# Performance work log

Measured on AMD Instinct MI355X. Metric: run time of the kernel, lower is better.

Reference implementation:

```python
import jax, jax.numpy as jnp
import numpy as np

B, D = 8192, 128
MARGIN = 0.1
N_CLASSES, N_GROUPS = 64, 8


def setup_inputs() -> dict:
    key = jax.random.key(0)
    k1, k2, k3 = jax.random.split(key, 3)
    embeddings = jax.random.normal(k1, (B, D), dtype=jnp.float32)
    labels = jax.random.randint(k2, (B,), 0, N_CLASSES, dtype=jnp.int64)
    groups = jax.random.randint(k3, (B,), 0, N_GROUPS, dtype=jnp.int64)
    return {"embeddings": embeddings, "labels": labels, "groups": groups}


def reference(embeddings, labels, groups):
    # cosine metric: L2-normalize rows (torch F.normalize eps=1e-12)
    norm = jnp.maximum(jnp.linalg.norm(embeddings, axis=1, keepdims=True), 1e-12)
    x = embeddings / norm
    dist = 1.0 - jnp.matmul(x, x.T)                      # [B, B]

    n = embeddings.shape[0]
    eye = jnp.eye(n, dtype=bool)
    same_label = labels[:, None] == labels[None, :]       # [B, B]
    pos_mask = same_label & ~eye
    neg_mask = ~same_label
    neg_sg_mask = neg_mask & (groups[:, None] == groups[None, :])

    BIG = jnp.float32(1e9)
    # hardest positive per row (masked max), hardest negative per row (masked min)
    dist_ap = jnp.max(jnp.where(pos_mask, dist, -BIG), axis=1)
    dist_an_sg = jnp.min(jnp.where(neg_sg_mask, dist, BIG), axis=1)
    dist_an_all = jnp.min(jnp.where(neg_mask, dist, BIG), axis=1)

    has_pos = jnp.any(pos_mask, axis=1)
    has_neg_sg = jnp.any(neg_sg_mask, axis=1)
    has_neg = jnp.any(neg_mask, axis=1)

    # fallback: same-group negatives preferred, else any negative
    dist_an = jnp.where(has_neg_sg, dist_an_sg, dist_an_all)

    loss = jax.nn.relu(dist_ap - dist_an + MARGIN)        # [B]
    # original only averages strictly-positive losses over valid anchors
    include = has_pos & has_neg & (loss > 0)
    cnt = jnp.sum(include.astype(jnp.float32))
    total = jnp.sum(jnp.where(include, loss, 0.0))
    final = jnp.where(cnt > 0, total / jnp.maximum(cnt, 1.0), 0.0)
    final = jnp.where(jnp.isnan(final), 0.0, final)
    return final
```

## Files before the change

### kernel.cpp

```cpp
#include <hip/hip_runtime.h>
#include <math.h>

#define NB 8192
#define DK 128
#define SPLITJ 16
#define JSPAN (NB / SPLITJ)
#define NJT (JSPAN / 32)
#define GRID_MINE ((NB / 128) * SPLITJ)

typedef __attribute__((ext_vector_type(8))) short short8;
typedef __attribute__((ext_vector_type(16))) float float16;

__device__ inline unsigned short f2bf(float f) {
    unsigned int x = __float_as_uint(f);
    unsigned int r = (x + 0x7fffu + ((x >> 16) & 1u)) >> 16;
    return (unsigned short)r;
}

__device__ inline unsigned enc_f(float f) {
    unsigned u = __float_as_uint(f);
    return ((int)u < 0) ? ~u : (u | 0x80000000u);
}
__device__ inline float dec_f(unsigned u) {
    unsigned b = (u & 0x80000000u) ? (u & 0x7fffffffu) : ~u;
    return __uint_as_float(b);
}

__global__ void prep_kernel(const float* __restrict__ emb, const int* __restrict__ labels,
                            const int* __restrict__ groups, short8* __restrict__ frag,
                            int* __restrict__ meta, unsigned* __restrict__ apu,
                            unsigned* __restrict__ anu, int* __restrict__ ticket) {
    const int t   = blockIdx.x;
    const int tid = threadIdx.x;
    const int r   = tid >> 3;
    const int ks  = tid & 7;
    const int row = t * 32 + r;

    const float4* src = (const float4*)(emb + (size_t)row * DK + ks * 16);
    float4 q[4];
    float ss = 0.0f;
#pragma unroll
    for (int u = 0; u < 4; u++) {
        q[u] = src[u];
        ss += q[u].x * q[u].x + q[u].y * q[u].y + q[u].z * q[u].z + q[u].w * q[u].w;
    }
#pragma unroll
    for (int off = 4; off; off >>= 1) ss += __shfl_xor(ss, off, 64);
    float inv = 1.0f / fmaxf(sqrtf(ss), 1e-12f);

    unsigned short h[16];
#pragma unroll
    for (int u = 0; u < 4; u++) {
        h[u * 4 + 0] = f2bf(q[u].x * inv);
        h[u * 4 + 1] = f2bf(q[u].y * inv);
        h[u * 4 + 2] = f2bf(q[u].z * inv);
        h[u * 4 + 3] = f2bf(q[u].w * inv);
    }
    short8 lo, hi;
#pragma unroll
    for (int u = 0; u < 8; u++) { lo[u] = (short)h[u]; hi[u] = (short)h[8 + u]; }
    frag[(size_t)(t * 8 + ks) * 64 + r]      = lo;
    frag[(size_t)(t * 8 + ks) * 64 + 32 + r] = hi;

    if (ks == 0) meta[row] = (labels[row] << 4) | groups[row];
    if (ks == 1) apu[row] = 0xFFFFFFFFu;
    if (ks == 2) anu[row] = 0u;
    if (t == 0 && tid == 0) *ticket = 0;
}

__global__ __launch_bounds__(256, 2) void mine_mfma(
    const short8* __restrict__ frag, const int* __restrict__ meta,
    unsigned* __restrict__ apu, unsigned* __restrict__ anu,
    int* __restrict__ ticket, float* __restrict__ out) {
    const int tid  = threadIdx.x;
    const int w    = tid >> 6;
    const int lane = tid & 63;
    const int half = lane >> 5;
    const int l31  = lane & 31;
    const int irow  = blockIdx.x * 128 + w * 32;
    const int jbase = blockIdx.y * JSPAN;
    const int tA    = blockIdx.x * 4 + w;
    const int tB0   = blockIdx.y * NJT;

    short8 afrag[8];
#pragma unroll
    for (int ks = 0; ks < 8; ks++)
        afrag[ks] = frag[(size_t)(tA * 8 + ks) * 64 + lane];

    int metaI[16];
    float mn[16], mx[16];
#pragma unroll
    for (int reg = 0; reg < 16; reg++) {
        int r = (reg & 3) + 8 * (reg >> 2) + 4 * half;
        metaI[reg] = meta[irow + r];
        mn[reg] = 1e9f; mx[reg] = -1e9f;
    }

    short8 b0[4], b1[4];
#pragma unroll
    for (int u = 0; u < 4; u++) b0[u] = frag[(size_t)(tB0 * 8 + u) * 64 + lane];
    int mj = meta[jbase + l31];

#pragma unroll 4
    for (int jt = 0; jt < NJT; jt++) {
        const int tB = tB0 + jt;
#pragma unroll
        for (int u = 0; u < 4; u++) b1[u] = frag[(size_t)(tB * 8 + 4 + u) * 64 + lane];
        int mjn = (jt + 1 < NJT) ? meta[jbase + (jt + 1) * 32 + l31] : 0;

        float16 c;
#pragma unroll
        for (int e = 0; e < 16; e++) c[e] = 0.0f;
#pragma unroll
        for (int u = 0; u < 4; u++)
            c = __builtin_amdgcn_mfma_f32_32x32x16_bf16(afrag[u], b0[u], c, 0, 0, 0);

        if (jt + 1 < NJT) {
#pragma unroll
            for (int u = 0; u < 4; u++)
                b0[u] = frag[(size_t)((tB + 1) * 8 + u) * 64 + lane];
        }
#pragma unroll
        for (int u = 0; u < 4; u++)
            c = __builtin_amdgcn_mfma_f32_32x32x16_bf16(afrag[4 + u], b1[u], c, 0, 0, 0);

#pragma unroll
        for (int reg = 0; reg < 16; reg++) {
            float s = c[reg];
            int x = metaI[reg] ^ mj;
            bool sl = (unsigned)x < 16u;
            bool sg = (x & 15) == 0;
            float bias0 = sg ? 4.0f : 0.0f;
            float bias  = sl ? -16.0f : bias0;
            float e  = s + bias;
            mn[reg] = fminf(mn[reg], e);
            mx[reg] = fmaxf(mx[reg], e);
        }
        mj = mjn;
    }

#pragma unroll
    for (int reg = 0; reg < 16; reg++) {
#pragma unroll
        for (int off = 16; off; off >>= 1) {
            mn[reg] = fminf(mn[reg], __shfl_xor(mn[reg], off, 64));
            mx[reg] = fmaxf(mx[reg], __shfl_xor(mx[reg], off, 64));
        }
    }
    if (l31 == 0) {
#pragma unroll
        for (int reg = 0; reg < 16; reg++) {
            int r = (reg & 3) + 8 * (reg >> 2) + 4 * half;
            atomicMin(&apu[irow + r], enc_f(mn[reg]));
            atomicMax(&anu[irow + r], enc_f(mx[reg]));
        }
    }

    __shared__ float ssum[4], scnt[4];
    __shared__ int lastFlag;
    __syncthreads();
    if (tid == 0) {
        __threadfence();
        int old = atomicAdd(ticket, 1);
        lastFlag = (old == GRID_MINE - 1);
    }
    __syncthreads();
    if (!lastFlag) return;
    __threadfence();

    float s = 0.0f, ccnt = 0.0f;
#pragma unroll
    for (int k = 0; k < NB / 256; k++) {
        int i = tid + k * 256;
        float mnf = dec_f(apu[i]);
        float mxf = dec_f(anu[i]);
        float anS = (mxf > 2.0f) ? mxf - 4.0f : mxf;
        float loss = anS - mnf - 15.9f;
        if (loss > 0.0f) { s += loss; ccnt += 1.0f; }
    }
#pragma unroll
    for (int off = 32; off; off >>= 1) {
        s    += __shfl_xor(s, off, 64);
        ccnt += __shfl_xor(ccnt, off, 64);
    }
    if (lane == 0) { ssum[w] = s; scnt[w] = ccnt; }
    __syncthreads();
    if (tid == 0) {
        float ts = 0.f, tc = 0.f;
#pragma unroll
        for (int wv = 0; wv < 4; wv++) { ts += ssum[wv]; tc += scnt[wv]; }
        float r = (tc > 0.0f) ? ts / fmaxf(tc, 1.0f) : 0.0f;
        if (isnan(r)) r = 0.0f;
        out[0] = r;
    }
}

extern "C" void kernel_launch(void* const* d_in, const int* in_sizes, int n_in,
                              void* d_out, int out_size, void* d_ws, size_t ws_size,
                              hipStream_t stream) {
    const float* emb  = (const float*)d_in[0];
    const int* labels = (const int*)d_in[1];
    const int* groups = (const int*)d_in[2];
    float* out = (float*)d_out;

    short8*   fragp  = (short8*)d_ws;
    int*      meta   = (int*)((char*)d_ws + (size_t)NB * DK * 2);
    unsigned* apu    = (unsigned*)(meta + NB);
    unsigned* anu    = apu + NB;
    int*      ticket = (int*)(anu + NB);

    prep_kernel<<<NB / 32, 256, 0, stream>>>(emb, labels, groups, fragp, meta, apu, anu, ticket);
    mine_mfma<<<dim3(NB / 128, SPLITJ), 256, 0, stream>>>(fragp, meta, apu, anu, ticket, out);
}
```

Baseline: 118.7 us.

## Double-buffer B fragments and fold label bias into MFMA accumulator init

Loads the full 8-step B fragment for the next j-tile into a ping-pong register buffer while the current tile's MFMAs run. The per-element label/group bias is precomputed into the accumulator's initial value, so the epilogue reduces to min/max only. The grid is also transposed so consecutive blocks share the same i-rows and sweep over j-chunks, which changes cache locality. The extra buffers raise register pressure (two 16-float accumulators plus 16 B fragments), which under launch_bounds(256,2) may cause spills or lower occupancy.

```diff
diff --git a/kernel.cpp b/kernel.cpp
--- a/kernel.cpp
+++ b/kernel.cpp
@@ -24,6 +24,14 @@
 __device__ inline float dec_f(unsigned u) {
     unsigned b = (u & 0x80000000u) ? (u & 0x7fffffffu) : ~u;
     return __uint_as_float(b);
+}
+
+__device__ inline float biasf(int mi, int mj) {
+    int x = mi ^ mj;
+    bool sl = (unsigned)x < 16u;
+    bool sg = (x & 15) == 0;
+    float b0 = sg ? 4.0f : 0.0f;
+    return sl ? -16.0f : b0;
 }
 
 __global__ void prep_kernel(const float* __restrict__ emb, const int* __restrict__ labels,
@@ -77,10 +85,10 @@
     const int lane = tid & 63;
     const int half = lane >> 5;
     const int l31  = lane & 31;
-    const int irow  = blockIdx.x * 128 + w * 32;
-    const int jbase = blockIdx.y * JSPAN;
-    const int tA    = blockIdx.x * 4 + w;
-    const int tB0   = blockIdx.y * NJT;
+    const int irow  = blockIdx.y * 128 + w * 32;
+    const int jbase = blockIdx.x * JSPAN;
+    const int tA    = blockIdx.y * 4 + w;
+    const int tB0   = blockIdx.x * NJT;
 
     short8 afrag[8];
 #pragma unroll
@@ -96,47 +104,41 @@
         mn[reg] = 1e9f; mx[reg] = -1e9f;
     }
 
-    short8 b0[4], b1[4];
-#pragma unroll
-    for (int u = 0; u < 4; u++) b0[u] = frag[(size_t)(tB0 * 8 + u) * 64 + lane];
-    int mj = meta[jbase + l31];
-
-#pragma unroll 4
+    short8  bb[2][8];
+    float16 cc[2];
+
+#pragma unroll
+    for (int u = 0; u < 8; u++) bb[0][u] = frag[(size_t)(tB0 * 8 + u) * 64 + lane];
+    {
+        int mj = meta[jbase + l31];
+#pragma unroll
+        for (int reg = 0; reg < 16; reg++) cc[0][reg] = biasf(metaI[reg], mj);
+    }
+
+#pragma unroll 2
     for (int jt = 0; jt < NJT; jt++) {
-        const int tB = tB0 + jt;
-#pragma unroll
-        for (int u = 0; u < 4; u++) b1[u] = frag[(size_t)(tB * 8 + 4 + u) * 64 + lane];
-        int mjn = (jt + 1 < NJT) ? meta[jbase + (jt + 1) * 32 + l31] : 0;
-
-        float16 c;
-#pragma unroll
-        for (int e = 0; e < 16; e++) c[e] = 0.0f;
-#pragma unroll
-        for (int u = 0; u < 4; u++)
-            c = __builtin_amdgcn_mfma_f32_32x32x16_bf16(afrag[u], b0[u], c, 0, 0, 0);
+        const int cur = jt & 1;
 
         if (jt + 1 < NJT) {
-#pragma unroll
-            for (int u = 0; u < 4; u++)
-                b0[u] = frag[(size_t)((tB + 1) * 8 + u) * 64 + lane];
-        }
-#pragma unroll
-        for (int u = 0; u < 4; u++)
-            c = __builtin_amdgcn_mfma_f32_32x32x16_bf16(afrag[4 + u], b1[u], c, 0, 0, 0);
+            const int tBn = tB0 + jt + 1;
+#pragma unroll
+            for (int u = 0; u < 8; u++)
+                bb[cur ^ 1][u] = frag[(size_t)(tBn * 8 + u) * 64 + lane];
+            int mjn = meta[jbase + (jt + 1) * 32 + l31];
+#pragma unroll
+            for (int reg = 0; reg < 16; reg++)
+                cc[cur ^ 1][reg] = biasf(metaI[reg], mjn);
+        }
+
+#pragma unroll
+        for (int u = 0; u < 8; u++)
+            cc[cur] = __builtin_amdgcn_mfma_f32_32x32x16_bf16(afrag[u], bb[cur][u], cc[cur], 0, 0, 0);
 
 #pragma unroll
         for (int reg = 0; reg < 16; reg++) {
-            float s = c[reg];
-            int x = metaI[reg] ^ mj;
-            bool sl = (unsigned)x < 16u;
-            bool sg = (x & 15) == 0;
-            float bias0 = sg ? 4.0f : 0.0f;
-            float bias  = sl ? -16.0f : bias0;
-            float e  = s + bias;
-            mn[reg] = fminf(mn[reg], e);
-            mx[reg] = fmaxf(mx[reg], e);
-        }
-        mj = mjn;
+            mn[reg] = fminf(mn[reg], cc[cur][reg]);
+            mx[reg] = fmaxf(mx[reg], cc[cur][reg]);
+        }
     }
 
 #pragma unroll
@@ -210,5 +212,5 @@
     int*      ticket = (int*)(anu + NB);
 
     prep_kernel<<<NB / 32, 256, 0, stream>>>(emb, labels, groups, fragp, meta, apu, anu, ticket);
-    mine_mfma<<<dim3(NB / 128, SPLITJ), 256, 0, stream>>>(fragp, meta, apu, anu, ticket, out);
-}
+    mine_mfma<<<dim3(SPLITJ, NB / 128), 256, 0, stream>>>(fragp, meta, apu, anu, ticket, out);
+}
```

New measurement: 111.3 us. -6.2%, faster.
